# Optimization experiments

Measured on AMD Instinct MI355X. Metric: run time of the kernel, lower is better.

## Reference

```python
import jax, jax.numpy as jnp
import numpy as np

N_E = 8192
DIM = 256
BETA = 0.25


def _l2norm(x, eps=1e-12):
    # matches F.normalize(p=2, dim=-1): x / max(||x||, eps)
    n = jnp.sqrt(jnp.sum(x * x, axis=-1, keepdims=True))
    return x / jnp.maximum(n, eps)


def setup_inputs() -> dict:
    key = jax.random.key(0)
    k1, k2 = jax.random.split(key)
    z = jax.random.normal(k1, (8, 1024, DIM), dtype=jnp.float32)
    embedding_weight = jax.random.normal(k2, (N_E, DIM), dtype=jnp.float32)
    return {"z": z, "embedding_weight": embedding_weight}


def reference(z, embedding_weight):
    z = _l2norm(z)                                   # [B,S,D]
    zf = z.reshape(-1, DIM)                          # [N,D]
    embed_norm = _l2norm(embedding_weight)           # [n_e,D]
    # d = ||z||^2 + ||e||^2 - 2 z.e  -> [N, n_e]
    d = (jnp.sum(zf * zf, axis=1, keepdims=True)
         + jnp.sum(embed_norm * embed_norm, axis=1)
         - 2.0 * jnp.einsum('bd,nd->bn', zf, embed_norm))
    encoding_indices = jnp.argmin(d, axis=1).reshape(z.shape[:-1])  # [B,S]
    z_q = embedding_weight[encoding_indices]          # gather raw codes
    z_q = _l2norm(z_q)                                # [B,S,D]
    loss = (BETA * jnp.mean((jax.lax.stop_gradient(z_q) - z) ** 2)
            + jnp.mean((z_q - jax.lax.stop_gradient(z)) ** 2))
    z_q = z + jax.lax.stop_gradient(z_q - z)          # straight-through
    return z_q, loss, encoding_indices
```

## Files before the change

kernel.cpp:

```cpp
#include <hip/hip_runtime.h>
#include <cfloat>
#include <math.h>

#define DIM    256
#define N_TOK  8192
#define N_E    8192
#define NSEG   512
#define MARGIN 0.008f

typedef __attribute__((ext_vector_type(8))) short bf16x8;
typedef __attribute__((ext_vector_type(4))) float f32x4;

__device__ __forceinline__ unsigned short f2bf(float f) {
    unsigned u = __float_as_uint(f);
    unsigned r = u + 0x7fff + ((u >> 16) & 1);
    return (unsigned short)(r >> 16);
}
__device__ __forceinline__ unsigned fkey(float f) {
    unsigned u = __float_as_uint(f);
    return (u & 0x80000000u) ? ~u : (u | 0x80000000u);
}

__global__ __launch_bounds__(256) void l2norm_all(const float* __restrict__ z,
                                                  const float* __restrict__ emb,
                                                  float* __restrict__ zn,
                                                  unsigned short* __restrict__ zb,
                                                  float* __restrict__ en,
                                                  unsigned short* __restrict__ eb,
                                                  float* __restrict__ e2) {
    const int lane = threadIdx.x & 63;
    const bool isE = blockIdx.x < (N_E / 4);
    const int row = (isE ? blockIdx.x : blockIdx.x - N_E / 4) * 4 + (threadIdx.x >> 6);
    const float* in = isE ? emb : z;
    float* out = isE ? en : zn;
    unsigned short* outb = isE ? eb : zb;
    const float4 v = *(const float4*)(in + row * DIM + lane * 4);
    float s = v.x * v.x + v.y * v.y + v.z * v.z + v.w * v.w;
#pragma unroll
    for (int off = 1; off < 64; off <<= 1) s += __shfl_xor(s, off, 64);
    const float inv = 1.0f / fmaxf(sqrtf(s), 1e-12f);
    const float4 o = make_float4(v.x * inv, v.y * inv, v.z * inv, v.w * inv);
    *(float4*)(out + row * DIM + lane * 4) = o;
    ushort4 ob; ob.x = f2bf(o.x); ob.y = f2bf(o.y); ob.z = f2bf(o.z); ob.w = f2bf(o.w);
    *(ushort4*)(outb + row * DIM + lane * 4) = ob;
    if (isE) {
        float q = o.x * o.x + o.y * o.y + o.z * o.z + o.w * o.w;
#pragma unroll
        for (int off = 1; off < 64; off <<= 1) q += __shfl_xor(q, off, 64);
        if (lane == 0) e2[row] = q;
    }
}

__global__ __launch_bounds__(256, 2) void mfma_dist(const unsigned short* __restrict__ zb,
                                                    const unsigned short* __restrict__ eb,
                                                    const float* __restrict__ e2,
                                                    float* __restrict__ segM) {
    __shared__ __align__(16) unsigned short As[2][128][32];
    __shared__ __align__(16) unsigned short Bs[2][128][32];
    __shared__ __align__(16) float sm[8][128];

    const int tid  = threadIdx.x;
    const int lane = tid & 63;
    const int wave = tid >> 6;
    const int wm = wave & 1, wn = wave >> 1;
    const int row0 = (blockIdx.x & 63) * 128;
    const int col0 = (blockIdx.x >> 6) * 128;
    const int fr = lane & 15, q = lane >> 4;

    f32x4 acc[4][4];
#pragma unroll
    for (int ci = 0; ci < 4; ci++)
#pragma unroll
        for (int zi = 0; zi < 4; zi++) acc[ci][zi] = (f32x4){0.f, 0.f, 0.f, 0.f};

    const int srow  = lane >> 2;
    const int skoff = (lane & 3) * 8;
    const unsigned short* gA = zb + (row0 + wave * 32 + srow) * DIM + skoff;
    const unsigned short* gB = eb + (col0 + wave * 32 + srow) * DIM + skoff;

    auto stage = [&](int buf, int kcn) {
#pragma unroll
        for (int j = 0; j < 2; j++) {
            __builtin_amdgcn_global_load_lds(
                (const __attribute__((address_space(1))) unsigned int*)(gA + j * 16 * DIM + kcn * 32),
                (__attribute__((address_space(3))) unsigned int*)&As[buf][wave * 32 + j * 16][0],
                16, 0, 0);
            __builtin_amdgcn_global_load_lds(
                (const __attribute__((address_space(1))) unsigned int*)(gB + j * 16 * DIM + kcn * 32),
                (__attribute__((address_space(3))) unsigned int*)&Bs[buf][wave * 32 + j * 16][0],
                16, 0, 0);
        }
    };
    auto compute = [&](int buf) {
        bf16x8 cf[4], zfr[4];
#pragma unroll
        for (int i = 0; i < 4; i++) cf[i]  = *(const bf16x8*)&Bs[buf][wn * 64 + i * 16 + fr][q * 8];
#pragma unroll
        for (int i = 0; i < 4; i++) zfr[i] = *(const bf16x8*)&As[buf][wm * 64 + i * 16 + fr][q * 8];
#pragma unroll
        for (int ci = 0; ci < 4; ci++)
#pragma unroll
            for (int zi = 0; zi < 4; zi++)
                acc[ci][zi] = __builtin_amdgcn_mfma_f32_16x16x32_bf16(cf[ci], zfr[zi], acc[ci][zi], 0, 0, 0);
    };

    stage(0, 0);
#pragma unroll
    for (int kc = 0; kc < 8; kc += 2) {
        __syncthreads();
        stage(1, kc + 1);
        compute(0);
        __syncthreads();
        if (kc + 2 < 8) stage(0, kc + 2);
        compute(1);
    }

    float4 e2q[4];
#pragma unroll
    for (int ci = 0; ci < 4; ci++)
        e2q[ci] = *(const float4*)&e2[col0 + wn * 64 + ci * 16 + q * 4];
#pragma unroll
    for (int ci = 0; ci < 4; ci++) {
#pragma unroll
        for (int zi = 0; zi < 4; zi++) {
            const float t0 = fmaf(-2.0f, acc[ci][zi][0], e2q[ci].x);
            const float t1 = fmaf(-2.0f, acc[ci][zi][1], e2q[ci].y);
            const float t2 = fmaf(-2.0f, acc[ci][zi][2], e2q[ci].z);
            const float t3 = fmaf(-2.0f, acc[ci][zi][3], e2q[ci].w);
            float mm = fminf(fminf(t0, t1), fminf(t2, t3));
            mm = fminf(mm, __shfl_xor(mm, 16, 64));
            mm = fminf(mm, __shfl_xor(mm, 32, 64));
            if (q == 0) sm[wn * 4 + ci][wm * 64 + zi * 16 + fr] = mm;
        }
    }
    __syncthreads();
    {
        const int rl = tid & 127, part = tid >> 7;
        float4 v;
        v.x = sm[part * 4 + 0][rl]; v.y = sm[part * 4 + 1][rl];
        v.z = sm[part * 4 + 2][rl]; v.w = sm[part * 4 + 3][rl];
        *(float4*)&segM[(size_t)(row0 + rl) * NSEG + (col0 >> 4) + part * 4] = v;
    }
}

__global__ __launch_bounds__(256) void select_rescore(const float* __restrict__ segM,
                                                      const float* __restrict__ en,
                                                      const float* __restrict__ e2,
                                                      float* zq,
                                                      float* out_base,
                                                      float* __restrict__ pl) {
    const int lane = threadIdx.x & 63;
    const int row  = (blockIdx.x << 2) + (threadIdx.x >> 6);
    const float4* p = (const float4*)(segM + (size_t)row * NSEG);
    const float4 v0 = p[lane];
    const float4 v1 = p[64 + lane];
    const float vv[8] = {v0.x, v0.y, v0.z, v0.w, v1.x, v1.y, v1.z, v1.w};
    float m = vv[0];
#pragma unroll
    for (int j = 1; j < 8; j++) m = fminf(m, vv[j]);
#pragma unroll
    for (int off = 1; off < 64; off <<= 1) m = fminf(m, __shfl_xor(m, off, 64));
    const float thr = m + MARGIN;

    const int q = lane >> 4, f = lane & 15;
    const float4* zp = (const float4*)(zq + (size_t)row * DIM);
    float4 z4[4];
#pragma unroll
    for (int j = 0; j < 4; j++) z4[j] = zp[j * 16 + f];

    unsigned long long pk = ~0ull;
#pragma unroll
    for (int j = 0; j < 8; j++) {
        unsigned long long bal = __ballot(vv[j] <= thr);
        while (bal) {
            const int l = __ffsll(bal) - 1;
            bal &= bal - 1;
            const int seg = (j < 4) ? (l * 4 + j) : (256 + l * 4 + (j - 4));
#pragma unroll
            for (int g = 0; g < 4; g++) {
                const int col = seg * 16 + g * 4 + q;
                const float4* ep = (const float4*)(en + (size_t)col * DIM);
                float s = 0.f;
#pragma unroll
                for (int jj = 0; jj < 4; jj++) {
                    const float4 ev = ep[jj * 16 + f];
                    s = fmaf(z4[jj].x, ev.x, s); s = fmaf(z4[jj].y, ev.y, s);
                    s = fmaf(z4[jj].z, ev.z, s); s = fmaf(z4[jj].w, ev.w, s);
                }
#pragma unroll
                for (int off = 1; off < 16; off <<= 1) s += __shfl_xor(s, off, 64);
                const float d = fmaf(-2.0f, s, e2[col]);
                const unsigned long long key =
                    ((unsigned long long)fkey(d) << 32) | (unsigned)col;
                if (key < pk) pk = key;
            }
        }
    }
#pragma unroll
    for (int off = 16; off < 64; off <<= 1) {
        const unsigned long long o = __shfl_xor(pk, off, 64);
        if (o < pk) pk = o;
    }
    const int i = (int)(pk & 0xffffffffu);

    const float4 qv = *(const float4*)(en + (size_t)i * DIM + lane * 4);
    const float4 zv = *(const float4*)(zq + (size_t)row * DIM + lane * 4);
    const float dx = qv.x - zv.x, dy = qv.y - zv.y, dz = qv.z - zv.z, dw = qv.w - zv.w;
    float s = dx * dx + dy * dy + dz * dz + dw * dw;
    *(float4*)(zq + (size_t)row * DIM + lane * 4) = qv;
#pragma unroll
    for (int off = 1; off < 64; off <<= 1) s += __shfl_xor(s, off, 64);
    if (lane == 0) {
        pl[row] = s;
        out_base[N_TOK * DIM + 1 + row] = (float)i;
    }
}

__global__ __launch_bounds__(1024) void finalize_loss(const float* __restrict__ pl,
                                                      float* __restrict__ out) {
    __shared__ float sw[16];
    const int t = threadIdx.x;
    float s = 0.f;
#pragma unroll
    for (int j = 0; j < 8; j++) s += pl[t + j * 1024];
#pragma unroll
    for (int off = 1; off < 64; off <<= 1) s += __shfl_xor(s, off, 64);
    if ((t & 63) == 0) sw[t >> 6] = s;
    __syncthreads();
    if (t < 16) {
        float v = sw[t];
#pragma unroll
        for (int off = 1; off < 16; off <<= 1) v += __shfl_xor(v, off, 64);
        if (t == 0) out[N_TOK * DIM] = v * (1.25f / 2097152.0f);
    }
}

extern "C" void kernel_launch(void* const* d_in, const int* in_sizes, int n_in,
                              void* d_out, int out_size, void* d_ws, size_t ws_size,
                              hipStream_t stream) {
    const float* z   = (const float*)d_in[0];
    const float* emb = (const float*)d_in[1];
    float* out = (float*)d_out;
    char* ws = (char*)d_ws;

    float*          en   = (float*)(ws);
    unsigned short* eb   = (unsigned short*)(ws + 8388608);
    unsigned short* zb   = (unsigned short*)(ws + 12582912);
    float*          e2   = (float*)(ws + 16777216);
    float*          segM = (float*)(ws + 16809984);
    float*          pl   = (float*)(ws + 33587200);

    l2norm_all<<<(N_E + N_TOK) / 4, 256, 0, stream>>>(z, emb, out, zb, en, eb, e2);
    mfma_dist<<<64 * 64, 256, 0, stream>>>(zb, eb, e2, segM);
    select_rescore<<<N_TOK / 4, 256, 0, stream>>>(segM, en, e2, out, out, pl);
    finalize_loss<<<1, 1024, 0, stream>>>(pl, out);
}
```

Before: 148.2 us.

## Pre-swizzle bf16 operands into MFMA fragment layout and store half-precision segment minima

The normalize kernel now writes bf16 z and codebook rows in a fragment-ordered layout, so the distance kernel loads MFMA operands straight from global memory into registers with double buffering, with no LDS staging or barriers. Segment minima now cover 8 codes instead of 16 and are stored as fp16, which halves the candidate re-scoring work per selected segment and keeps the intermediate buffer the same size. The margin is widened to absorb fp16 rounding, which risks more candidates being re-scored. Occupancy is raised to 3 blocks per SIMD.

Measured after the change: 160.6 us. 1.08x slower.

```diff
diff --git a/kernel.cpp b/kernel.cpp
--- a/kernel.cpp
+++ b/kernel.cpp
@@ -1,15 +1,17 @@
 #include <hip/hip_runtime.h>
+#include <hip/hip_fp16.h>
 #include <cfloat>
 #include <math.h>
 
 #define DIM    256
 #define N_TOK  8192
 #define N_E    8192
-#define NSEG   512
-#define MARGIN 0.008f
+#define NSEG   1024
+#define MARGIN 0.012f
 
 typedef __attribute__((ext_vector_type(8))) short bf16x8;
 typedef __attribute__((ext_vector_type(4))) float f32x4;
+typedef __attribute__((ext_vector_type(8))) unsigned short ushort8;
 
 __device__ __forceinline__ unsigned short f2bf(float f) {
     unsigned u = __float_as_uint(f);
@@ -20,20 +22,28 @@
     unsigned u = __float_as_uint(f);
     return (u & 0x80000000u) ? ~u : (u | 0x80000000u);
 }
+__device__ __forceinline__ unsigned short f2h(float f) {
+    const __half h = __float2half(f);
+    return *(const unsigned short*)&h;
+}
+__device__ __forceinline__ float h2f(unsigned short u) {
+    __half_raw r; r.x = u;
+    return __half2float((__half)r);
+}
 
 __global__ __launch_bounds__(256) void l2norm_all(const float* __restrict__ z,
                                                   const float* __restrict__ emb,
                                                   float* __restrict__ zn,
-                                                  unsigned short* __restrict__ zb,
+                                                  unsigned short* __restrict__ zsw,
                                                   float* __restrict__ en,
-                                                  unsigned short* __restrict__ eb,
+                                                  unsigned short* __restrict__ esw,
                                                   float* __restrict__ e2) {
     const int lane = threadIdx.x & 63;
     const bool isE = blockIdx.x < (N_E / 4);
     const int row = (isE ? blockIdx.x : blockIdx.x - N_E / 4) * 4 + (threadIdx.x >> 6);
     const float* in = isE ? emb : z;
     float* out = isE ? en : zn;
-    unsigned short* outb = isE ? eb : zb;
+    unsigned short* outb = isE ? esw : zsw;
     const float4 v = *(const float4*)(in + row * DIM + lane * 4);
     float s = v.x * v.x + v.y * v.y + v.z * v.z + v.w * v.w;
 #pragma unroll
@@ -42,7 +52,12 @@
     const float4 o = make_float4(v.x * inv, v.y * inv, v.z * inv, v.w * inv);
     *(float4*)(out + row * DIM + lane * 4) = o;
     ushort4 ob; ob.x = f2bf(o.x); ob.y = f2bf(o.y); ob.z = f2bf(o.z); ob.w = f2bf(o.w);
-    *(ushort4*)(outb + row * DIM + lane * 4) = ob;
+    {
+        const int k0 = lane * 4;
+        const size_t sidx = ((size_t)((row >> 4) * 8 + (k0 >> 5)) * 64
+                             + ((k0 >> 3) & 3) * 16 + (row & 15)) * 8 + (k0 & 7);
+        *(ushort4*)(outb + sidx) = ob;
+    }
     if (isE) {
         float q = o.x * o.x + o.y * o.y + o.z * o.z + o.w * o.w;
 #pragma unroll
@@ -51,13 +66,11 @@
     }
 }
 
-__global__ __launch_bounds__(256, 2) void mfma_dist(const unsigned short* __restrict__ zb,
-                                                    const unsigned short* __restrict__ eb,
+__global__ __launch_bounds__(256, 3) void mfma_dist(const unsigned short* __restrict__ zsw,
+                                                    const unsigned short* __restrict__ esw,
                                                     const float* __restrict__ e2,
-                                                    float* __restrict__ segM) {
-    __shared__ __align__(16) unsigned short As[2][128][32];
-    __shared__ __align__(16) unsigned short Bs[2][128][32];
-    __shared__ __align__(16) float sm[8][128];
+                                                    unsigned short* __restrict__ segMh) {
+    __shared__ float sm[16][128];
 
     const int tid  = threadIdx.x;
     const int lane = tid & 63;
@@ -73,46 +86,30 @@
 #pragma unroll
         for (int zi = 0; zi < 4; zi++) acc[ci][zi] = (f32x4){0.f, 0.f, 0.f, 0.f};
 
-    const int srow  = lane >> 2;
-    const int skoff = (lane & 3) * 8;
-    const unsigned short* gA = zb + (row0 + wave * 32 + srow) * DIM + skoff;
-    const unsigned short* gB = eb + (col0 + wave * 32 + srow) * DIM + skoff;
-
-    auto stage = [&](int buf, int kcn) {
-#pragma unroll
-        for (int j = 0; j < 2; j++) {
-            __builtin_amdgcn_global_load_lds(
-                (const __attribute__((address_space(1))) unsigned int*)(gA + j * 16 * DIM + kcn * 32),
-                (__attribute__((address_space(3))) unsigned int*)&As[buf][wave * 32 + j * 16][0],
-                16, 0, 0);
-            __builtin_amdgcn_global_load_lds(
-                (const __attribute__((address_space(1))) unsigned int*)(gB + j * 16 * DIM + kcn * 32),
-                (__attribute__((address_space(3))) unsigned int*)&Bs[buf][wave * 32 + j * 16][0],
-                16, 0, 0);
+    const int aBase = (col0 >> 4) + wn * 4;
+    const int bBase = (row0 >> 4) + wm * 4;
+    auto la = [&](int i, int kc) {
+        return *(const bf16x8*)(esw + (size_t)(aBase + i) * 4096 + kc * 512 + lane * 8);
+    };
+    auto lb = [&](int i, int kc) {
+        return *(const bf16x8*)(zsw + (size_t)(bBase + i) * 4096 + kc * 512 + lane * 8);
+    };
+
+    bf16x8 ca[2][4], zb[2][4];
+#pragma unroll
+    for (int i = 0; i < 4; i++) { ca[0][i] = la(i, 0); zb[0][i] = lb(i, 0); }
+#pragma unroll
+    for (int kc = 0; kc < 8; kc++) {
+        const int cur = kc & 1, nxt = cur ^ 1;
+        if (kc < 7) {
+#pragma unroll
+            for (int i = 0; i < 4; i++) { ca[nxt][i] = la(i, kc + 1); zb[nxt][i] = lb(i, kc + 1); }
         }
-    };
-    auto compute = [&](int buf) {
-        bf16x8 cf[4], zfr[4];
-#pragma unroll
-        for (int i = 0; i < 4; i++) cf[i]  = *(const bf16x8*)&Bs[buf][wn * 64 + i * 16 + fr][q * 8];
-#pragma unroll
-        for (int i = 0; i < 4; i++) zfr[i] = *(const bf16x8*)&As[buf][wm * 64 + i * 16 + fr][q * 8];
 #pragma unroll
         for (int ci = 0; ci < 4; ci++)
 #pragma unroll
             for (int zi = 0; zi < 4; zi++)
-                acc[ci][zi] = __builtin_amdgcn_mfma_f32_16x16x32_bf16(cf[ci], zfr[zi], acc[ci][zi], 0, 0, 0);
-    };
-
-    stage(0, 0);
-#pragma unroll
-    for (int kc = 0; kc < 8; kc += 2) {
-        __syncthreads();
-        stage(1, kc + 1);
-        compute(0);
-        __syncthreads();
-        if (kc + 2 < 8) stage(0, kc + 2);
-        compute(1);
+                acc[ci][zi] = __builtin_amdgcn_mfma_f32_16x16x32_bf16(ca[cur][ci], zb[cur][zi], acc[ci][zi], 0, 0, 0);
     }
 
     float4 e2q[4];
@@ -129,21 +126,21 @@
             const float t3 = fmaf(-2.0f, acc[ci][zi][3], e2q[ci].w);
             float mm = fminf(fminf(t0, t1), fminf(t2, t3));
             mm = fminf(mm, __shfl_xor(mm, 16, 64));
-            mm = fminf(mm, __shfl_xor(mm, 32, 64));
-            if (q == 0) sm[wn * 4 + ci][wm * 64 + zi * 16 + fr] = mm;
+            if (q == 0) sm[wn * 8 + ci * 2 + 0][wm * 64 + zi * 16 + fr] = mm;
+            if (q == 2) sm[wn * 8 + ci * 2 + 1][wm * 64 + zi * 16 + fr] = mm;
         }
     }
     __syncthreads();
     {
         const int rl = tid & 127, part = tid >> 7;
-        float4 v;
-        v.x = sm[part * 4 + 0][rl]; v.y = sm[part * 4 + 1][rl];
-        v.z = sm[part * 4 + 2][rl]; v.w = sm[part * 4 + 3][rl];
-        *(float4*)&segM[(size_t)(row0 + rl) * NSEG + (col0 >> 4) + part * 4] = v;
-    }
-}
-
-__global__ __launch_bounds__(256) void select_rescore(const float* __restrict__ segM,
+        ushort8 o8;
+#pragma unroll
+        for (int j = 0; j < 8; j++) o8[j] = f2h(sm[part * 8 + j][rl]);
+        *(ushort8*)&segMh[(size_t)(row0 + rl) * NSEG + (col0 >> 3) + part * 8] = o8;
+    }
+}
+
+__global__ __launch_bounds__(256) void select_rescore(const unsigned short* __restrict__ segMh,
                                                       const float* __restrict__ en,
                                                       const float* __restrict__ e2,
                                                       float* zq,
@@ -151,13 +148,15 @@
                                                       float* __restrict__ pl) {
     const int lane = threadIdx.x & 63;
     const int row  = (blockIdx.x << 2) + (threadIdx.x >> 6);
-    const float4* p = (const float4*)(segM + (size_t)row * NSEG);
-    const float4 v0 = p[lane];
-    const float4 v1 = p[64 + lane];
-    const float vv[8] = {v0.x, v0.y, v0.z, v0.w, v1.x, v1.y, v1.z, v1.w};
+    const unsigned short* ph = segMh + (size_t)row * NSEG + lane * 16;
+    const ushort8 u0 = *(const ushort8*)ph;
+    const ushort8 u1 = *(const ushort8*)(ph + 8);
+    float vv[16];
+#pragma unroll
+    for (int j = 0; j < 8; j++) { vv[j] = h2f(u0[j]); vv[8 + j] = h2f(u1[j]); }
     float m = vv[0];
 #pragma unroll
-    for (int j = 1; j < 8; j++) m = fminf(m, vv[j]);
+    for (int j = 1; j < 16; j++) m = fminf(m, vv[j]);
 #pragma unroll
     for (int off = 1; off < 64; off <<= 1) m = fminf(m, __shfl_xor(m, off, 64));
     const float thr = m + MARGIN;
@@ -170,15 +169,15 @@
 
     unsigned long long pk = ~0ull;
 #pragma unroll
-    for (int j = 0; j < 8; j++) {
+    for (int j = 0; j < 16; j++) {
         unsigned long long bal = __ballot(vv[j] <= thr);
         while (bal) {
             const int l = __ffsll(bal) - 1;
             bal &= bal - 1;
-            const int seg = (j < 4) ? (l * 4 + j) : (256 + l * 4 + (j - 4));
-#pragma unroll
-            for (int g = 0; g < 4; g++) {
-                const int col = seg * 16 + g * 4 + q;
+            const int seg = l * 16 + j;
+#pragma unroll
+            for (int g = 0; g < 2; g++) {
+                const int col = seg * 8 + g * 4 + q;
                 const float4* ep = (const float4*)(en + (size_t)col * DIM);
                 float s = 0.f;
 #pragma unroll
@@ -243,15 +242,15 @@
     float* out = (float*)d_out;
     char* ws = (char*)d_ws;
 
-    float*          en   = (float*)(ws);
-    unsigned short* eb   = (unsigned short*)(ws + 8388608);
-    unsigned short* zb   = (unsigned short*)(ws + 12582912);
-    float*          e2   = (float*)(ws + 16777216);
-    float*          segM = (float*)(ws + 16809984);
-    float*          pl   = (float*)(ws + 33587200);
-
-    l2norm_all<<<(N_E + N_TOK) / 4, 256, 0, stream>>>(z, emb, out, zb, en, eb, e2);
-    mfma_dist<<<64 * 64, 256, 0, stream>>>(zb, eb, e2, segM);
-    select_rescore<<<N_TOK / 4, 256, 0, stream>>>(segM, en, e2, out, out, pl);
+    float*          en    = (float*)(ws);
+    unsigned short* esw   = (unsigned short*)(ws + 8388608);
+    unsigned short* zsw   = (unsigned short*)(ws + 12582912);
+    float*          e2    = (float*)(ws + 16777216);
+    unsigned short* segMh = (unsigned short*)(ws + 16809984);
+    float*          pl    = (float*)(ws + 33587200);
+
+    l2norm_all<<<(N_E + N_TOK) / 4, 256, 0, stream>>>(z, emb, out, zsw, en, esw, e2);
+    mfma_dist<<<64 * 64, 256, 0, stream>>>(zsw, esw, e2, segMh);
+    select_rescore<<<N_TOK / 4, 256, 0, stream>>>(segMh, en, e2, out, out, pl);
     finalize_loss<<<1, 1024, 0, stream>>>(pl, out);
 }
```
